# Kernel optimization log

Hardware: AMD Instinct MI355X
Metric: run time of the kernel (lower is better)

Reference implementation:

```python
import jax, jax.numpy as jnp
import numpy as np

N, E = 100000, 600000
IN, HID, OUT, ED = 128, 128, 64, 32


def _gine_conv(x, src, dst, edge_feats, We, be, Wa, ba, Wb, bb):
    # GINEConv: msg = relu(x_j + Linear(edge_attr)); out = MLP((1+eps)*x + sum msg), eps=0
    e = edge_feats @ We + be                      # [E, C]
    msg = jax.nn.relu(x[src] + e)                 # gather + edge-add
    agg = jax.ops.segment_sum(msg, dst, num_segments=x.shape[0])
    h = x + agg                                   # eps = 0
    return jax.nn.relu(h @ Wa + ba) @ Wb + bb     # 2-layer MLP


def setup_inputs() -> dict:
    key = jax.random.key(0)
    ks = jax.random.split(key, 20)
    g = lambda k, shp, fan: jax.random.normal(k, shp, jnp.float32) * (1.0 / np.sqrt(fan))
    return {
        "x": jax.random.normal(ks[0], (N, IN), jnp.float32),
        "edge_index": jax.random.randint(ks[1], (2, E), 0, N, dtype=jnp.int32),
        "edge_feats": jax.random.normal(ks[2], (E, ED), jnp.float32),
        # conv1: edge lin (ED->IN), nn1 (IN->HID->HID)
        "We1": g(ks[3], (ED, IN), ED), "be1": jnp.zeros((IN,), jnp.float32),
        "W1a": g(ks[4], (IN, HID), IN), "b1a": jnp.zeros((HID,), jnp.float32),
        "W1b": g(ks[5], (HID, HID), HID), "b1b": jnp.zeros((HID,), jnp.float32),
        # conv2: edge lin (ED->HID), nn2 (HID->HID->HID)
        "We2": g(ks[6], (ED, HID), ED), "be2": jnp.zeros((HID,), jnp.float32),
        "W2a": g(ks[7], (HID, HID), HID), "b2a": jnp.zeros((HID,), jnp.float32),
        "W2b": g(ks[8], (HID, HID), HID), "b2b": jnp.zeros((HID,), jnp.float32),
        # heads
        "Wfc1": g(ks[9], (HID, HID), HID), "bfc1": jnp.zeros((HID,), jnp.float32),
        "Wfc2": g(ks[10], (HID, OUT), HID), "bfc2": jnp.zeros((OUT,), jnp.float32),
    }


def reference(x, edge_index, edge_feats,
              We1, be1, W1a, b1a, W1b, b1b,
              We2, be2, W2a, b2a, W2b, b2b,
              Wfc1, bfc1, Wfc2, bfc2):
    src, dst = edge_index[0], edge_index[1]  # source_to_target flow
    h = _gine_conv(x, src, dst, edge_feats, We1, be1, W1a, b1a, W1b, b1b)
    h = jnp.tanh(h)                          # dropout: eval-mode identity
    h = _gine_conv(h, src, dst, edge_feats, We2, be2, W2a, b2a, W2b, b2b)
    h = jnp.tanh(h)
    h = jnp.tanh(h @ Wfc1 + bfc1)
    return h @ Wfc2 + bfc2
```

## Files before the change

### kernel.cpp

```cpp
#include <hip/hip_runtime.h>
#include <hip/hip_fp16.h>
#include <math.h>

#define N_NODES 100000
#define N_EDGES 600000
#define NB_SCAN ((N_NODES + 1023) / 1024)

typedef unsigned short u16;
typedef __bf16 bf16x8 __attribute__((ext_vector_type(8)));
typedef float  f32x4  __attribute__((ext_vector_type(4)));

__device__ __forceinline__ u16 f2bf(float f) {
    union { float f; unsigned u; } c; c.f = f;
    unsigned u = c.u + 0x7fffu + ((c.u >> 16) & 1u);
    return (u16)(u >> 16);
}
__device__ __forceinline__ float bf2f(u16 h) {
    union { unsigned u; float f; } c; c.u = ((unsigned)h) << 16;
    return c.f;
}
__device__ __forceinline__ float fast_tanh(float x) {
    float e = __expf(2.0f * x);
    return 1.0f - 2.0f * __builtin_amdgcn_rcpf(e + 1.0f);
}

__global__ void hist_k(const int* __restrict__ dst, int* __restrict__ counts,
                       int* __restrict__ rank)
{
    int e = blockIdx.x * 256 + threadIdx.x;
    if (e < N_EDGES) rank[e] = atomicAdd(&counts[dst[e]], 1);
}

__global__ void scan_a_k(const int* __restrict__ counts, int* __restrict__ row_ptr,
                         int* __restrict__ blockSums)
{
    __shared__ int s[256];
    const int t = threadIdx.x;
    const int base = blockIdx.x * 1024 + t * 4;
    int c[4];
#pragma unroll
    for (int j = 0; j < 4; ++j) c[j] = (base + j < N_NODES) ? counts[base + j] : 0;
    const int tot = c[0] + c[1] + c[2] + c[3];
    s[t] = tot;
    __syncthreads();
    for (int off = 1; off < 256; off <<= 1) {
        int v = (t >= off) ? s[t - off] : 0;
        __syncthreads();
        s[t] += v;
        __syncthreads();
    }
    int run = s[t] - tot;
#pragma unroll
    for (int j = 0; j < 4; ++j) {
        if (base + j < N_NODES) row_ptr[base + j] = run;
        run += c[j];
    }
    if (t == 255) blockSums[blockIdx.x] = s[255];
}

__global__ void scan_b_k(const int* __restrict__ blockSums, int* __restrict__ blockOffs)
{
    if (threadIdx.x == 0) {
        int run = 0;
        for (int b = 0; b < NB_SCAN; ++b) { blockOffs[b] = run; run += blockSums[b]; }
    }
}

__global__ void scan_c_k(int* __restrict__ row_ptr, const int* __restrict__ blockOffs)
{
    int i = blockIdx.x * 256 + threadIdx.x;
    if (i < N_NODES) row_ptr[i] += blockOffs[i >> 10];
    if (i == 0) row_ptr[N_NODES] = N_EDGES;
}

__global__ void scatter_k(const int* __restrict__ src, const int* __restrict__ dst,
                          const int* __restrict__ row_ptr, const int* __restrict__ rank,
                          int* __restrict__ perm, int* __restrict__ src_sorted,
                          int* __restrict__ dst_sorted)
{
    int e = blockIdx.x * 256 + threadIdx.x;
    if (e < N_EDGES) {
        int pos = row_ptr[dst[e]] + rank[e];
        perm[pos] = e;
        src_sorted[pos] = src[e];
        dst_sorted[pos] = dst[e];
    }
}

__global__ void wprep_k(const float* __restrict__ W1a, const float* __restrict__ W1b,
                        const float* __restrict__ W2a, const float* __restrict__ W2b,
                        const float* __restrict__ Wf1, const float* __restrict__ Wf2,
                        const float* __restrict__ We1, const float* __restrict__ We2,
                        u16* __restrict__ wT)
{
    int idx = blockIdx.x * 256 + threadIdx.x;
    if (idx >= 98304) return;
    if (idx >= 90112) {
        int l = idx - 90112;
        const int m = l >> 12;
        l &= 4095;
        const float* src = m ? We2 : We1;
        const int k = l >> 7, n = l & 127;
        const float w = src[k * 128 + n];
        const u16 hi = f2bf(w);
        const u16 lo = f2bf(w - bf2f(hi));
        const int base = 180224 + m * 8192;
        wT[base + n * 32 + k]        = hi;
        wT[base + 4096 + n * 32 + k] = lo;
        return;
    }
    int m, local;
    if      (idx < 16384) { m = 0; local = idx; }
    else if (idx < 32768) { m = 1; local = idx - 16384; }
    else if (idx < 49152) { m = 2; local = idx - 32768; }
    else if (idx < 65536) { m = 3; local = idx - 49152; }
    else if (idx < 81920) { m = 4; local = idx - 65536; }
    else                  { m = 5; local = idx - 81920; }
    const int N = (m == 5) ? 64 : 128;
    const float* src = (m == 0) ? W1a : (m == 1) ? W1b : (m == 2) ? W2a
                     : (m == 3) ? W2b : (m == 4) ? Wf1 : Wf2;
    const int k = local / N, n = local % N;
    const float w = src[k * N + n];
    const u16 hi = f2bf(w);
    const u16 lo = f2bf(w - bf2f(hi));
    const int base = m * 32768;
    const int sz   = (m == 5) ? 8192 : 16384;
    wT[base + n * 128 + k]      = hi;
    wT[base + sz + n * 128 + k] = lo;
}

__global__ __launch_bounds__(256, 6) void fused_conv_k(
    const float* __restrict__ x, const float* __restrict__ ef,
    const int* __restrict__ perm, const int* __restrict__ src_s,
    const int* __restrict__ dst_s, const int* __restrict__ row_ptr,
    const u16* __restrict__ WeT_hi, const u16* __restrict__ WeT_lo,
    const float* __restrict__ be, float* __restrict__ agg)
{
    __shared__ __align__(16) char smem[16896];
    u16 (*efHi)[40]  = (u16 (*)[40])smem;
    u16 (*efLo)[40]  = (u16 (*)[40])(smem + 5120);
    u16 (*msg16)[132] = (u16 (*)[132])smem;
    __shared__ int sSrc[64];
    __shared__ int sDst[64];

    const int t  = threadIdx.x;
    const int i0 = blockIdx.x * 64;

    if (t < 64) { sSrc[t] = src_s[i0 + t]; sDst[t] = dst_s[i0 + t]; }
    {
        const int row = t >> 2;
        const int q   = t & 3;
        const int e   = perm[i0 + row];
        const float* p = ef + (size_t)e * 32 + q * 8;
        const float4 v0 = *(const float4*)(p);
        const float4 v1 = *(const float4*)(p + 4);
        const float vv[8] = {v0.x, v0.y, v0.z, v0.w, v1.x, v1.y, v1.z, v1.w};
        unsigned hp[4], lp[4];
#pragma unroll
        for (int i = 0; i < 4; ++i) {
            const u16 h0 = f2bf(vv[2 * i]),     h1 = f2bf(vv[2 * i + 1]);
            const u16 l0 = f2bf(vv[2 * i]     - bf2f(h0));
            const u16 l1 = f2bf(vv[2 * i + 1] - bf2f(h1));
            hp[i] = (unsigned)h0 | ((unsigned)h1 << 16);
            lp[i] = (unsigned)l0 | ((unsigned)l1 << 16);
        }
        *(uint4*)&efHi[row][q * 8] = make_uint4(hp[0], hp[1], hp[2], hp[3]);
        *(uint4*)&efLo[row][q * 8] = make_uint4(lp[0], lp[1], lp[2], lp[3]);
    }
    __syncthreads();

    const int lane = t & 63, wave = t >> 6;
    const int quad = lane >> 4, col = lane & 15;

    bf16x8 bHi[2], bLo[2];
#pragma unroll
    for (int j = 0; j < 2; ++j) {
        const int nt = wave * 2 + j;
        const size_t off = (size_t)(nt * 16 + col) * 32 + quad * 8;
        bHi[j] = *(const bf16x8*)(WeT_hi + off);
        bLo[j] = *(const bf16x8*)(WeT_lo + off);
    }

    float xv[2][4][4];
#pragma unroll
    for (int m = 0; m < 4; ++m)
#pragma unroll
        for (int r = 0; r < 4; ++r) {
            const int s = sSrc[m * 16 + quad * 4 + r];
            const float* xp = x + (size_t)s * 128 + wave * 32 + col;
            xv[0][m][r] = xp[0];
            xv[1][m][r] = xp[16];
        }

    f32x4 acc[2][4];
#pragma unroll
    for (int j = 0; j < 2; ++j) {
        const float bv = be[wave * 32 + j * 16 + col];
#pragma unroll
        for (int m = 0; m < 4; ++m) acc[j][m] = (f32x4){bv, bv, bv, bv};
    }
#pragma unroll
    for (int m = 0; m < 4; ++m) {
        const bf16x8 aHi = *(const bf16x8*)&efHi[m * 16 + col][quad * 8];
        const bf16x8 aLo = *(const bf16x8*)&efLo[m * 16 + col][quad * 8];
#pragma unroll
        for (int j = 0; j < 2; ++j) {
            acc[j][m] = __builtin_amdgcn_mfma_f32_16x16x32_bf16(aHi, bHi[j], acc[j][m], 0, 0, 0);
            acc[j][m] = __builtin_amdgcn_mfma_f32_16x16x32_bf16(aHi, bLo[j], acc[j][m], 0, 0, 0);
            acc[j][m] = __builtin_amdgcn_mfma_f32_16x16x32_bf16(aLo, bHi[j], acc[j][m], 0, 0, 0);
        }
    }

#pragma unroll
    for (int j = 0; j < 2; ++j)
#pragma unroll
        for (int m = 0; m < 4; ++m)
#pragma unroll
            for (int r = 0; r < 4; ++r)
                acc[j][m][r] = fmaxf(acc[j][m][r] + xv[j][m][r], 0.f);

    __syncthreads();
#pragma unroll
    for (int j = 0; j < 2; ++j)
#pragma unroll
        for (int m = 0; m < 4; ++m)
#pragma unroll
            for (int r = 0; r < 4; ++r) {
                const __half hv = __float2half_rn(acc[j][m][r]);
                msg16[m * 16 + quad * 4 + r][wave * 32 + j * 16 + col] =
                    *(const u16*)&hv;
            }
    __syncthreads();

    const int c2 = lane * 2;
    const int nF = sDst[0], nL = sDst[63];
    for (int n = nF + wave; n <= nL; n += 4) {
        const int rs = row_ptr[n];
        const int re = row_ptr[n + 1];
        const int lo = rs > i0 ? rs : i0;
        const int hi = re < i0 + 64 ? re : i0 + 64;
        float a0 = 0.f, a1 = 0.f;
        for (int i = lo; i < hi; ++i) {
            const __half2 v = *(const __half2*)(&msg16[i - i0][c2]);
            const float2 f = __half22float2(v);
            a0 += f.x; a1 += f.y;
        }
        float* dp = agg + (size_t)n * 128 + c2;
        const bool interior = (rs >= i0) && (re <= i0 + 64);
        if (interior) {
            *(float2*)dp = make_float2(a0, a1);
        } else if (hi > lo) {
            atomicAdd(dp,     a0);
            atomicAdd(dp + 1, a1);
        }
    }
}

template <int NT2, bool TANH1, bool TANHF, bool ADDAGG>
__global__ __launch_bounds__(256, 4) void mlp2_mfma_k(
    const float* __restrict__ xin, const float* __restrict__ agg,
    const u16* __restrict__ WaT_hi, const u16* __restrict__ WaT_lo,
    const float* __restrict__ ba,
    const u16* __restrict__ WbT_hi, const u16* __restrict__ WbT_lo,
    const float* __restrict__ bb,
    float* __restrict__ out)
{
    __shared__ u16 sHi[64][136];
    __shared__ u16 sLo[64][136];
    const int tid = threadIdx.x;
    const int n0  = blockIdx.x * 64;

    {
        const int mrow = tid >> 5, kq = tid & 31;
#pragma unroll
        for (int g = 0; g < 8; ++g) {
            const int row  = g * 8 + mrow;
            const int node = n0 + row;
            float4 v = make_float4(0.f, 0.f, 0.f, 0.f);
            if (node < N_NODES) {
                v = *(const float4*)(xin + (size_t)node * 128 + kq * 4);
                if (ADDAGG) {
                    float4 a4 = *(const float4*)(agg + (size_t)node * 128 + kq * 4);
                    v.x += a4.x; v.y += a4.y; v.z += a4.z; v.w += a4.w;
                }
            }
            const u16 h0 = f2bf(v.x), h1 = f2bf(v.y), h2 = f2bf(v.z), h3 = f2bf(v.w);
            const u16 l0 = f2bf(v.x - bf2f(h0)), l1 = f2bf(v.y - bf2f(h1));
            const u16 l2 = f2bf(v.z - bf2f(h2)), l3 = f2bf(v.w - bf2f(h3));
            *(uint2*)&sHi[row][kq * 4] =
                make_uint2((unsigned)h0 | ((unsigned)h1 << 16), (unsigned)h2 | ((unsigned)h3 << 16));
            *(uint2*)&sLo[row][kq * 4] =
                make_uint2((unsigned)l0 | ((unsigned)l1 << 16), (unsigned)l2 | ((unsigned)l3 << 16));
        }
    }
    __syncthreads();

    const int lane = tid & 63, wave = tid >> 6;
    const int quad = lane >> 4, col = lane & 15;

    f32x4 accA[2][4];
#pragma unroll
    for (int j = 0; j < 2; ++j) {
        const int nt = wave * 2 + j;
        const float bv = ba[nt * 16 + col];
#pragma unroll
        for (int m = 0; m < 4; ++m) accA[j][m] = (f32x4){bv, bv, bv, bv};

        bf16x8 bHi[4], bLo[4];
#pragma unroll
        for (int k0 = 0; k0 < 4; ++k0) {
            const size_t off = (size_t)(nt * 16 + col) * 128 + k0 * 32 + quad * 8;
            bHi[k0] = *(const bf16x8*)(WaT_hi + off);
            bLo[k0] = *(const bf16x8*)(WaT_lo + off);
        }
#pragma unroll 2
        for (int m = 0; m < 4; ++m) {
#pragma unroll
            for (int k0 = 0; k0 < 4; ++k0) {
                const bf16x8 aHi = *(const bf16x8*)&sHi[m * 16 + col][k0 * 32 + quad * 8];
                const bf16x8 aLo = *(const bf16x8*)&sLo[m * 16 + col][k0 * 32 + quad * 8];
                accA[j][m] = __builtin_amdgcn_mfma_f32_16x16x32_bf16(aHi, bHi[k0], accA[j][m], 0, 0, 0);
                accA[j][m] = __builtin_amdgcn_mfma_f32_16x16x32_bf16(aHi, bLo[k0], accA[j][m], 0, 0, 0);
                accA[j][m] = __builtin_amdgcn_mfma_f32_16x16x32_bf16(aLo, bHi[k0], accA[j][m], 0, 0, 0);
            }
        }
    }
    __syncthreads();

#pragma unroll
    for (int j = 0; j < 2; ++j) {
        const int ct = (wave * 2 + j) * 16 + col;
#pragma unroll
        for (int m = 0; m < 4; ++m) {
#pragma unroll
            for (int r = 0; r < 4; ++r) {
                float v = TANH1 ? fast_tanh(accA[j][m][r]) : fmaxf(accA[j][m][r], 0.f);
                const u16 hv = f2bf(v);
                const u16 lv = f2bf(v - bf2f(hv));
                const int row = m * 16 + quad * 4 + r;
                sHi[row][ct] = hv;
                sLo[row][ct] = lv;
            }
        }
    }
    __syncthreads();

    constexpr int JB   = NT2 / 4;
    constexpr int NOUT = NT2 * 16;
#pragma unroll
    for (int j = 0; j < JB; ++j) {
        const int nt = wave * JB + j;
        const float bv = bb[nt * 16 + col];
        f32x4 accB[4];
#pragma unroll
        for (int m = 0; m < 4; ++m) accB[m] = (f32x4){bv, bv, bv, bv};

        bf16x8 bHi[4], bLo[4];
#pragma unroll
        for (int k0 = 0; k0 < 4; ++k0) {
            const size_t off = (size_t)(nt * 16 + col) * 128 + k0 * 32 + quad * 8;
            bHi[k0] = *(const bf16x8*)(WbT_hi + off);
            bLo[k0] = *(const bf16x8*)(WbT_lo + off);
        }
#pragma unroll 2
        for (int m = 0; m < 4; ++m) {
#pragma unroll
            for (int k0 = 0; k0 < 4; ++k0) {
                const bf16x8 tHi = *(const bf16x8*)&sHi[m * 16 + col][k0 * 32 + quad * 8];
                const bf16x8 tLo = *(const bf16x8*)&sLo[m * 16 + col][k0 * 32 + quad * 8];
                accB[m] = __builtin_amdgcn_mfma_f32_16x16x32_bf16(tHi, bHi[k0], accB[m], 0, 0, 0);
                accB[m] = __builtin_amdgcn_mfma_f32_16x16x32_bf16(tHi, bLo[k0], accB[m], 0, 0, 0);
                accB[m] = __builtin_amdgcn_mfma_f32_16x16x32_bf16(tLo, bHi[k0], accB[m], 0, 0, 0);
            }
        }
#pragma unroll
        for (int m = 0; m < 4; ++m) {
#pragma unroll
            for (int r = 0; r < 4; ++r) {
                const int node = n0 + m * 16 + quad * 4 + r;
                if (node < N_NODES) {
                    float v = accB[m][r];
                    if (TANHF) v = fast_tanh(v);
                    out[(size_t)node * NOUT + nt * 16 + col] = v;
                }
            }
        }
    }
}

extern "C" void kernel_launch(void* const* d_in, const int* in_sizes, int n_in,
                              void* d_out, int out_size, void* d_ws, size_t ws_size,
                              hipStream_t stream)
{
    const float* x   = (const float*)d_in[0];
    const int*   ei  = (const int*)  d_in[1];
    const float* ef  = (const float*)d_in[2];
    const float* We1 = (const float*)d_in[3];
    const float* be1 = (const float*)d_in[4];
    const float* W1a = (const float*)d_in[5];
    const float* b1a = (const float*)d_in[6];
    const float* W1b = (const float*)d_in[7];
    const float* b1b = (const float*)d_in[8];
    const float* We2 = (const float*)d_in[9];
    const float* be2 = (const float*)d_in[10];
    const float* W2a = (const float*)d_in[11];
    const float* b2a = (const float*)d_in[12];
    const float* W2b = (const float*)d_in[13];
    const float* b2b = (const float*)d_in[14];
    const float* Wf1 = (const float*)d_in[15];
    const float* bf1 = (const float*)d_in[16];
    const float* Wf2 = (const float*)d_in[17];
    const float* bf2 = (const float*)d_in[18];
    float* out = (float*)d_out;

    const int* src = ei;
    const int* dst = ei + N_EDGES;

    float*  agg     = (float*)d_ws;
    float*  h       = agg + (size_t)N_NODES * 128;
    int*    row_ptr = (int*)(h + (size_t)N_NODES * 128);
    int*    perm    = row_ptr + (N_NODES + 8);
    int*    src_s   = perm + N_EDGES;
    int*    dst_srt = src_s + N_EDGES;
    u16*    wT      = (u16*)(dst_srt + N_EDGES);
    int* counts    = (int*)agg;
    int* rank      = counts + N_NODES;
    int* blockSums = rank + N_EDGES;
    int* blockOffs = blockSums + NB_SCAN;

    u16* W1aT = wT;
    u16* W1bT = wT + 32768;
    u16* W2aT = wT + 65536;
    u16* W2bT = wT + 98304;
    u16* Wf1T = wT + 131072;
    u16* Wf2T = wT + 163840;
    u16* We1T = wT + 180224;
    u16* We2T = wT + 188416;

    const int mlpGrid = (N_NODES + 63) / 64;
    const int eGrid   = (N_EDGES + 255) / 256;
    const int nGrid   = (N_NODES + 255) / 256;
    const int fcGrid  = N_EDGES / 64;
    const int wpGrid  = (98304 + 255) / 256;

    hipMemsetAsync(counts, 0, (size_t)N_NODES * sizeof(int), stream);
    hist_k   <<<eGrid,   256, 0, stream>>>(dst, counts, rank);
    wprep_k  <<<wpGrid,  256, 0, stream>>>(W1a, W1b, W2a, W2b, Wf1, Wf2, We1, We2, wT);
    scan_a_k <<<NB_SCAN, 256, 0, stream>>>(counts, row_ptr, blockSums);
    scan_b_k <<<1,        64, 0, stream>>>(blockSums, blockOffs);
    scan_c_k <<<nGrid,   256, 0, stream>>>(row_ptr, blockOffs);
    scatter_k<<<eGrid,   256, 0, stream>>>(src, dst, row_ptr, rank, perm, src_s, dst_srt);

    hipMemsetAsync(agg, 0, (size_t)N_NODES * 128 * sizeof(float), stream);
    fused_conv_k<<<fcGrid, 256, 0, stream>>>(x, ef, perm, src_s, dst_srt, row_ptr,
                                             We1T, We1T + 4096, be1, agg);
    mlp2_mfma_k<8, false, true, true><<<mlpGrid, 256, 0, stream>>>(
        x, agg, W1aT, W1aT + 16384, b1a, W1bT, W1bT + 16384, b1b, h);

    hipMemsetAsync(agg, 0, (size_t)N_NODES * 128 * sizeof(float), stream);
    fused_conv_k<<<fcGrid, 256, 0, stream>>>(h, ef, perm, src_s, dst_srt, row_ptr,
                                             We2T, We2T + 4096, be2, agg);
    mlp2_mfma_k<8, false, true, true><<<mlpGrid, 256, 0, stream>>>(
        h, agg, W2aT, W2aT + 16384, b2a, W2bT, W2bT + 16384, b2b, h);

    mlp2_mfma_k<4, true, false, false><<<mlpGrid, 256, 0, stream>>>(
        h, nullptr, Wf1T, Wf1T + 16384, bf1, Wf2T, Wf2T + 8192, bf2, out);
}
```

Before: 534.3 us.

## Fuse conv2 MLP with output heads and zero only boundary agg rows

Replaces the last two MLP kernels with a single kernel that runs four chained layers (conv2 MLP, tanh, fc1 with tanh, fc2) while keeping activations in shared memory. This avoids writing the intermediate h to global memory and reading it back. The full memset of agg is also replaced by a kernel that zeroes only rows whose edge ranges cross a 64-edge tile boundary or have no edges, on the assumption that the fused conv writes interior rows directly. That assumption ties correctness to how fused_conv_k writes its results.

```diff
diff --git a/kernel.cpp b/kernel.cpp
--- a/kernel.cpp
+++ b/kernel.cpp
@@ -84,6 +84,19 @@
         perm[pos] = e;
         src_sorted[pos] = src[e];
         dst_sorted[pos] = dst[e];
+    }
+}
+
+__global__ void nzero_k(const int* __restrict__ row_ptr, float* __restrict__ agg)
+{
+    const int idx = blockIdx.x * 256 + threadIdx.x;
+    const int n = idx >> 5;
+    if (n >= N_NODES) return;
+    const int rs = row_ptr[n], re = row_ptr[n + 1];
+    const bool interior = (rs < re) && ((rs >> 6) == ((re - 1) >> 6));
+    if (!interior) {
+        const int c = (idx & 31) * 4;
+        *(float4*)(agg + (size_t)n * 128 + c) = make_float4(0.f, 0.f, 0.f, 0.f);
     }
 }
 
@@ -383,6 +396,137 @@
                     if (TANHF) v = fast_tanh(v);
                     out[(size_t)node * NOUT + nt * 16 + col] = v;
                 }
+            }
+        }
+    }
+}
+
+__global__ __launch_bounds__(256, 4) void mlp4_mfma_k(
+    const float* __restrict__ xin, const float* __restrict__ agg,
+    const u16* __restrict__ W0hi, const u16* __restrict__ W0lo, const float* __restrict__ b0,
+    const u16* __restrict__ W1hi, const u16* __restrict__ W1lo, const float* __restrict__ b1,
+    const u16* __restrict__ W2hi, const u16* __restrict__ W2lo, const float* __restrict__ b2,
+    const u16* __restrict__ W3hi, const u16* __restrict__ W3lo, const float* __restrict__ b3,
+    float* __restrict__ out)
+{
+    __shared__ u16 sHi[64][136];
+    __shared__ u16 sLo[64][136];
+    const int tid = threadIdx.x;
+    const int n0  = blockIdx.x * 64;
+
+    {
+        const int mrow = tid >> 5, kq = tid & 31;
+#pragma unroll
+        for (int g = 0; g < 8; ++g) {
+            const int row  = g * 8 + mrow;
+            const int node = n0 + row;
+            float4 v = make_float4(0.f, 0.f, 0.f, 0.f);
+            if (node < N_NODES) {
+                v = *(const float4*)(xin + (size_t)node * 128 + kq * 4);
+                float4 a4 = *(const float4*)(agg + (size_t)node * 128 + kq * 4);
+                v.x += a4.x; v.y += a4.y; v.z += a4.z; v.w += a4.w;
+            }
+            const u16 h0 = f2bf(v.x), h1 = f2bf(v.y), h2 = f2bf(v.z), h3 = f2bf(v.w);
+            const u16 l0 = f2bf(v.x - bf2f(h0)), l1 = f2bf(v.y - bf2f(h1));
+            const u16 l2 = f2bf(v.z - bf2f(h2)), l3 = f2bf(v.w - bf2f(h3));
+            *(uint2*)&sHi[row][kq * 4] =
+                make_uint2((unsigned)h0 | ((unsigned)h1 << 16), (unsigned)h2 | ((unsigned)h3 << 16));
+            *(uint2*)&sLo[row][kq * 4] =
+                make_uint2((unsigned)l0 | ((unsigned)l1 << 16), (unsigned)l2 | ((unsigned)l3 << 16));
+        }
+    }
+    __syncthreads();
+
+    const int lane = tid & 63, wave = tid >> 6;
+    const int quad = lane >> 4, col = lane & 15;
+
+#pragma unroll 1
+    for (int l = 0; l < 3; ++l) {
+        const u16*   Whi = (l == 0) ? W0hi : (l == 1) ? W1hi : W2hi;
+        const u16*   Wlo = (l == 0) ? W0lo : (l == 1) ? W1lo : W2lo;
+        const float* bs  = (l == 0) ? b0   : (l == 1) ? b1   : b2;
+
+        f32x4 acc[2][4];
+#pragma unroll
+        for (int j = 0; j < 2; ++j) {
+            const int nt = wave * 2 + j;
+            const float bv = bs[nt * 16 + col];
+#pragma unroll
+            for (int m = 0; m < 4; ++m) acc[j][m] = (f32x4){bv, bv, bv, bv};
+
+            bf16x8 bHi[4], bLo[4];
+#pragma unroll
+            for (int k0 = 0; k0 < 4; ++k0) {
+                const size_t off = (size_t)(nt * 16 + col) * 128 + k0 * 32 + quad * 8;
+                bHi[k0] = *(const bf16x8*)(Whi + off);
+                bLo[k0] = *(const bf16x8*)(Wlo + off);
+            }
+#pragma unroll 2
+            for (int m = 0; m < 4; ++m) {
+#pragma unroll
+                for (int k0 = 0; k0 < 4; ++k0) {
+                    const bf16x8 aHi = *(const bf16x8*)&sHi[m * 16 + col][k0 * 32 + quad * 8];
+                    const bf16x8 aLo = *(const bf16x8*)&sLo[m * 16 + col][k0 * 32 + quad * 8];
+                    acc[j][m] = __builtin_amdgcn_mfma_f32_16x16x32_bf16(aHi, bHi[k0], acc[j][m], 0, 0, 0);
+                    acc[j][m] = __builtin_amdgcn_mfma_f32_16x16x32_bf16(aHi, bLo[k0], acc[j][m], 0, 0, 0);
+                    acc[j][m] = __builtin_amdgcn_mfma_f32_16x16x32_bf16(aLo, bHi[k0], acc[j][m], 0, 0, 0);
+                }
+            }
+        }
+        __syncthreads();
+
+#pragma unroll
+        for (int j = 0; j < 2; ++j) {
+            const int ct = (wave * 2 + j) * 16 + col;
+#pragma unroll
+            for (int m = 0; m < 4; ++m) {
+#pragma unroll
+                for (int r = 0; r < 4; ++r) {
+                    float v = (l == 0) ? fmaxf(acc[j][m][r], 0.f)
+                                       : fast_tanh(acc[j][m][r]);
+                    const u16 hv = f2bf(v);
+                    const u16 lv = f2bf(v - bf2f(hv));
+                    const int row = m * 16 + quad * 4 + r;
+                    sHi[row][ct] = hv;
+                    sLo[row][ct] = lv;
+                }
+            }
+        }
+        __syncthreads();
+    }
+
+    {
+        const int nt = wave;
+        const float bv = b3[nt * 16 + col];
+        f32x4 acc[4];
+#pragma unroll
+        for (int m = 0; m < 4; ++m) acc[m] = (f32x4){bv, bv, bv, bv};
+
+        bf16x8 bHi[4], bLo[4];
+#pragma unroll
+        for (int k0 = 0; k0 < 4; ++k0) {
+            const size_t off = (size_t)(nt * 16 + col) * 128 + k0 * 32 + quad * 8;
+            bHi[k0] = *(const bf16x8*)(W3hi + off);
+            bLo[k0] = *(const bf16x8*)(W3lo + off);
+        }
+#pragma unroll 2
+        for (int m = 0; m < 4; ++m) {
+#pragma unroll
+            for (int k0 = 0; k0 < 4; ++k0) {
+                const bf16x8 tHi = *(const bf16x8*)&sHi[m * 16 + col][k0 * 32 + quad * 8];
+                const bf16x8 tLo = *(const bf16x8*)&sLo[m * 16 + col][k0 * 32 + quad * 8];
+                acc[m] = __builtin_amdgcn_mfma_f32_16x16x32_bf16(tHi, bHi[k0], acc[m], 0, 0, 0);
+                acc[m] = __builtin_amdgcn_mfma_f32_16x16x32_bf16(tHi, bLo[k0], acc[m], 0, 0, 0);
+                acc[m] = __builtin_amdgcn_mfma_f32_16x16x32_bf16(tLo, bHi[k0], acc[m], 0, 0, 0);
+            }
+        }
+#pragma unroll
+        for (int m = 0; m < 4; ++m) {
+#pragma unroll
+            for (int r = 0; r < 4; ++r) {
+                const int node = n0 + m * 16 + quad * 4 + r;
+                if (node < N_NODES)
+                    out[(size_t)node * 64 + nt * 16 + col] = acc[m][r];
             }
         }
     }
@@ -442,6 +586,7 @@
     const int nGrid   = (N_NODES + 255) / 256;
     const int fcGrid  = N_EDGES / 64;
     const int wpGrid  = (98304 + 255) / 256;
+    const int nzGrid  = (N_NODES * 32 + 255) / 256;
 
     hipMemsetAsync(counts, 0, (size_t)N_NODES * sizeof(int), stream);
     hist_k   <<<eGrid,   256, 0, stream>>>(dst, counts, rank);
@@ -451,18 +596,20 @@
     scan_c_k <<<nGrid,   256, 0, stream>>>(row_ptr, blockOffs);
     scatter_k<<<eGrid,   256, 0, stream>>>(src, dst, row_ptr, rank, perm, src_s, dst_srt);
 
-    hipMemsetAsync(agg, 0, (size_t)N_NODES * 128 * sizeof(float), stream);
+    nzero_k<<<nzGrid, 256, 0, stream>>>(row_ptr, agg);
     fused_conv_k<<<fcGrid, 256, 0, stream>>>(x, ef, perm, src_s, dst_srt, row_ptr,
                                              We1T, We1T + 4096, be1, agg);
     mlp2_mfma_k<8, false, true, true><<<mlpGrid, 256, 0, stream>>>(
         x, agg, W1aT, W1aT + 16384, b1a, W1bT, W1bT + 16384, b1b, h);
 
-    hipMemsetAsync(agg, 0, (size_t)N_NODES * 128 * sizeof(float), stream);
+    nzero_k<<<nzGrid, 256, 0, stream>>>(row_ptr, agg);
     fused_conv_k<<<fcGrid, 256, 0, stream>>>(h, ef, perm, src_s, dst_srt, row_ptr,
                                              We2T, We2T + 4096, be2, agg);
-    mlp2_mfma_k<8, false, true, true><<<mlpGrid, 256, 0, stream>>>(
-        h, agg, W2aT, W2aT + 16384, b2a, W2bT, W2bT + 16384, b2b, h);
-
-    mlp2_mfma_k<4, true, false, false><<<mlpGrid, 256, 0, stream>>>(
-        h, nullptr, Wf1T, Wf1T + 16384, bf1, Wf2T, Wf2T + 8192, bf2, out);
-}
+    mlp4_mfma_k<<<mlpGrid, 256, 0, stream>>>(
+        h, agg,
+        W2aT, W2aT + 16384, b2a,
+        W2bT, W2bT + 16384, b2b,
+        Wf1T, Wf1T + 16384, bf1,
+        Wf2T, Wf2T + 8192,  bf2,
+        out);
+}
```

New measurement: 508.2 us. 1.05x faster.
